# Kernel optimization log

Hardware: AMD Instinct MI355X
Metric: run time of the kernel (lower is better)

The kernel has to match this reference:

```python
import jax, jax.numpy as jnp
import numpy as np

K = 16  # kNN neighbors (KnnEncoder default)


def _bn(h, g, s):
    # eval-mode BatchNorm with running mean 0 / var 1 folded into affine
    return h * g + s


def setup_inputs() -> dict:
    key = jax.random.key(0)
    cnt = [0]
    def nk():
        cnt[0] += 1
        return jax.random.fold_in(key, cnt[0])
    B, N = 4, 4096
    def W(i, o):
        return jax.random.normal(nk(), (i, o), jnp.float32) / np.float32(i) ** 0.5
    def bias(d):
        return jnp.zeros((d,), jnp.float32)
    def gamma(d):
        return jnp.ones((d,), jnp.float32) + 0.1 * jax.random.normal(nk(), (d,), jnp.float32)
    def beta(d):
        return 0.1 * jax.random.normal(nk(), (d,), jnp.float32)
    inp = dict(
        pos=jax.random.normal(nk(), (B, N, 3), jnp.float32),
        query_point_idx=jax.random.randint(nk(), (B,), 0, N),
        # PointNetConv local MLP: 6 -> 64 -> 128 -> 256 (plain last)
        cw1=W(6, 64), cb1=bias(64), cg1=gamma(64), cs1=beta(64),
        cw2=W(64, 128), cb2=bias(128), cg2=gamma(128), cs2=beta(128),
        cw3=W(128, 256), cb3=bias(256),
        # GlobalSAModule MLP: 259 -> 256 -> 512 -> 1024 (plain last)
        sw1=W(259, 256), sb1=bias(256), sg1=gamma(256), ss1=beta(256),
        sw2=W(256, 512), sb2=bias(512), sg2=gamma(512), ss2=beta(512),
        sw3=W(512, 1024), sb3=bias(1024),
        # EdgeGraspPredictor: 1280 -> 512 -> 256 -> 16
        pw1=W(1280, 512), pb1=bias(512),
        pw2=W(512, 256), pb2=bias(256),
        pw3=W(256, 16), pb3=bias(16),
    )
    return inp


def reference(pos, query_point_idx, cw1, cb1, cg1, cs1, cw2, cb2, cg2, cs2, cw3, cb3,
              sw1, sb1, sg1, ss1, sw2, sb2, sg2, ss2, sw3, sb3,
              pw1, pb1, pw2, pb2, pw3, pb3):
    B, N, _ = pos.shape
    # kNN within each cloud (self included, as torch_geometric knn with x==y)
    d2 = jnp.sum((pos[:, :, None, :] - pos[:, None, :, :]) ** 2, axis=-1)  # [B,N,N]
    _, idx = jax.lax.top_k(-d2, K)  # [B,N,K] targets for each source point n
    nbr = jax.vmap(lambda p, i: p[i])(pos, idx)  # [B,N,K,3] target positions
    # PointNetConv message: cat([x_j = pos_src, pos_src - pos_tgt])
    src = jnp.broadcast_to(pos[:, :, None, :], (B, N, K, 3))
    h = jnp.concatenate([src, src - nbr], axis=-1)  # [B,N,K,6]
    h = jnp.maximum(_bn(h @ cw1 + cb1, cg1, cs1), 0.0)
    h = jnp.maximum(_bn(h @ cw2 + cb2, cg2, cs2), 0.0)
    m = h @ cw3 + cb3  # [B,N,K,256] per-edge messages
    # scatter-max aggregation at target nodes (every node has its self edge)
    tgt = (idx + (jnp.arange(B) * N)[:, None, None]).reshape(-1)
    x = jax.ops.segment_max(m.reshape(-1, m.shape[-1]), tgt, num_segments=B * N)
    x = x.reshape(B, N, -1)  # [B,N,256] per-point features
    # GlobalSAModule: pointwise MLP then global max pool per cloud
    g = jnp.concatenate([x, pos], axis=-1)  # [B,N,259]
    g = jnp.maximum(_bn(g @ sw1 + sb1, sg1, ss1), 0.0)
    g = jnp.maximum(_bn(g @ sw2 + sb2, sg2, ss2), 0.0)
    g = g @ sw3 + sb3  # [B,N,1024]
    scene = jnp.max(g, axis=1)  # [B,1024]
    # gather query point feature, concat with scene feature, predictor MLP
    q = query_point_idx + jnp.arange(B) * N
    point_feat = x.reshape(B * N, -1)[q]  # [B,256]
    ef = jnp.concatenate([point_feat, scene], axis=-1)  # [B,1280]
    h = jnp.maximum(ef @ pw1 + pb1, 0.0)
    h = jnp.maximum(h @ pw2 + pb2, 0.0)
    return h @ pw3 + pb3  # [B,16]
```

## Files before the change

kernel.cpp:

```cpp
#include <hip/hip_runtime.h>

#define BB 4
#define NN 4096
#define KK 16

typedef unsigned short u16;
typedef unsigned int   u32;
typedef unsigned long long u64;

typedef __attribute__((ext_vector_type(8))) short bf16x8;
typedef __attribute__((ext_vector_type(4))) float f32x4;

__device__ __forceinline__ float b2f(u16 x){ return __uint_as_float(((u32)x) << 16); }
__device__ __forceinline__ u16 f2b(float f){
    u32 u = __float_as_uint(f);
    u32 r = (u + 0x7FFFu + ((u >> 16) & 1u)) >> 16;
    return (u16)r;
}
__device__ __forceinline__ u32 fmap(float f){
    u32 u = __float_as_uint(f);
    return (u & 0x80000000u) ? ~u : (u | 0x80000000u);
}
__device__ __forceinline__ float funmap(u32 u){
    u32 v = (u & 0x80000000u) ? (u ^ 0x80000000u) : ~u;
    return __uint_as_float(v);
}

#define N_ARR 27
__device__ const int ASZ[N_ARR] = {
    49152, 384, 64, 64, 64, 8192, 128, 128, 128, 32768, 256,
    66304, 256, 256, 256, 131072, 512, 512, 512, 524288, 1024,
    655360, 512, 131072, 256, 4096, 16 };
__device__ const int AOFF[N_ARR] = {
    0, 49152, 49536, 49600, 49664, 49728, 57920, 58048, 58176, 58304, 91072,
    91328, 157632, 157888, 158144, 158400, 289472, 289984, 290496, 291008, 815296,
    816320, 1471680, 1472192, 1603264, 1603520, 1607616 };

struct Ptrs { const void* p[N_ARR]; };

#define O_POS 0
#define O_CW1 49152
#define O_CB1 49536
#define O_CG1 49600
#define O_CS1 49664
#define O_CW2 49728
#define O_CB2 57920
#define O_CG2 58048
#define O_CS2 58176
#define O_CW3 58304
#define O_CB3 91072
#define O_SW1 91328
#define O_SB1 157632
#define O_SG1 157888
#define O_SS1 158144
#define O_SW2 158400
#define O_SB2 289472
#define O_SG2 289984
#define O_SS2 290496
#define O_SW3 291008
#define O_SB3 815296
#define O_PW1 816320
#define O_PB1 1471680
#define O_PW2 1472192
#define O_PB2 1603264
#define O_PW3 1603520
#define O_PB3 1607616

__global__ void detect_kernel(const u16* __restrict__ pos_u16, u32* __restrict__ flag){
    __shared__ int cnt;
    if (threadIdx.x == 0) cnt = 0;
    __syncthreads();
    int c = 0;
    #pragma unroll
    for (int s = 0; s < 4; ++s){
        u16 u = pos_u16[2*(threadIdx.x*4 + s)];
        int e = (u >> 7) & 0xFF;
        c += (e >= 0x68 && e <= 0x82) ? 1 : 0;
    }
    atomicAdd(&cnt, c);
    __syncthreads();
    if (threadIdx.x == 0) *flag = (cnt >= 512) ? 1u : 0u;
}

__device__ __forceinline__ void pack_one_src(const void* __restrict__ src, bool isbf,
                                             u16* __restrict__ dst, int tot, int log2n,
                                             int g, int T){
    const int nmask = (1 << log2n) - 1;
    for (int id = g; id < tot; id += T){
        int i = id & 7, lg = (id >> 3) & 3;
        int rest = id >> 5;
        int n = rest & nmask;
        int ks = rest >> log2n;
        int si = (ks*32 + lg*8 + i) << log2n | n;
        dst[id] = isbf ? ((const u16*)src)[si] : f2b(((const float*)src)[si]);
    }
}

__global__ __launch_bounds__(256) void prep_kernel(Ptrs pt, const u32* __restrict__ flagp,
        float* __restrict__ dst,
        u16* __restrict__ wp2, u16* __restrict__ wp3,
        u16* __restrict__ swp1, u16* __restrict__ swp2, u16* __restrict__ swp3){
    const bool isbf = (*flagp != 0);
    const int T = gridDim.x * 256;
    const int g = blockIdx.x * 256 + threadIdx.x;
    #pragma unroll
    for (int a = 0; a < N_ARR; ++a){
        const int sz = ASZ[a], off = AOFF[a];
        if (isbf){
            const u16* s = (const u16*)pt.p[a];
            for (int i = g; i < sz; i += T) dst[off + i] = b2f(s[i]);
        } else {
            const float* s = (const float*)pt.p[a];
            for (int i = g; i < sz; i += T) dst[off + i] = s[i];
        }
    }
    pack_one_src(pt.p[5],  isbf, wp2,    8192,  7, g, T);
    pack_one_src(pt.p[9],  isbf, wp3,   32768,  8, g, T);
    pack_one_src(pt.p[11], isbf, swp1,  65536,  8, g, T);
    pack_one_src(pt.p[15], isbf, swp2, 131072,  9, g, T);
    pack_one_src(pt.p[19], isbf, swp3, 524288, 10, g, T);
}

#define QCAP 192
__device__ __forceinline__ void refine16(u64* __restrict__ buf, int& cnt, float& tau, int lane){
    u64 loc[3];
    #pragma unroll
    for (int q = 0; q < 3; ++q){
        int p = lane + (q << 6);
        loc[q] = (p < cnt) ? buf[p] : ~0ull;
    }
    u64 m = ~0ull;
    #pragma unroll
    for (int r = 0; r < KK; ++r){
        m = loc[0];
        m = loc[1] < m ? loc[1] : m;
        m = loc[2] < m ? loc[2] : m;
        #pragma unroll
        for (int off = 32; off > 0; off >>= 1){
            u64 o = __shfl_xor(m, off);
            m = o < m ? o : m;
        }
        if (lane == r) buf[r] = m;
        #pragma unroll
        for (int q = 0; q < 3; ++q) if (loc[q] == m) loc[q] = ~0ull;
    }
    cnt = KK;
    tau = __uint_as_float((u32)(m >> 32));
}

__global__ __launch_bounds__(512) void knn_kernel(const float* __restrict__ conv,
                                                  int* __restrict__ knn_out,
                                                  u32* __restrict__ deg){
    __shared__ __align__(16) u64 kbuf[16*QCAP];
    const int b  = blockIdx.x >> 8;
    const int i0 = (blockIdx.x & 255) << 4;
    const float* pb = conv + O_POS + (size_t)b*NN*3;
    const int tid = threadIdx.x;
    const int lane = tid & 63;
    const int wv = tid >> 6;
    const int iA = i0 + wv*2, iB = iA + 1;
    const float ax = pb[3*iA], ay = pb[3*iA+1], az = pb[3*iA+2];
    const float bx = pb[3*iB], by = pb[3*iB+1], bz = pb[3*iB+2];
    u64* bufA = kbuf + (wv*2)*QCAP;
    u64* bufB = bufA + QCAP;

    float tauA = 3.0e38f, tauB = 3.0e38f;
    int cntA = 0, cntB = 0;
    for (int t = 0; t < 64; t += 4){
        float cx[4], cy[4], cz[4];
        #pragma unroll
        for (int c = 0; c < 4; ++c){
            int j = lane + ((t + c) << 6);
            const float* p = pb + 3*j;
            cx[c] = p[0]; cy[c] = p[1]; cz[c] = p[2];
        }
        #pragma unroll
        for (int c = 0; c < 4; ++c){
            int j = lane + ((t + c) << 6);
            float dxA = ax - cx[c], dyA = ay - cy[c], dzA = az - cz[c];
            float d2A = __fadd_rn(__fadd_rn(__fmul_rn(dxA,dxA), __fmul_rn(dyA,dyA)), __fmul_rn(dzA,dzA));
            float dxB = bx - cx[c], dyB = by - cy[c], dzB = bz - cz[c];
            float d2B = __fadd_rn(__fadd_rn(__fmul_rn(dxB,dxB), __fmul_rn(dyB,dyB)), __fmul_rn(dzB,dzB));
            bool pA = (d2A <= tauA);
            u64 balA = __ballot(pA);
            if (balA){
                int nins = __popcll(balA);
                if (cntA + nins > QCAP) refine16(bufA, cntA, tauA, lane);
                if (pA){
                    int ofs = __popcll(balA & ((1ull << lane) - 1ull));
                    bufA[cntA + ofs] = (((u64)__float_as_uint(d2A)) << 32) | (u32)j;
                }
                cntA += nins;
            }
            bool pB = (d2B <= tauB);
            u64 balB = __ballot(pB);
            if (balB){
                int nins = __popcll(balB);
                if (cntB + nins > QCAP) refine16(bufB, cntB, tauB, lane);
                if (pB){
                    int ofs = __popcll(balB & ((1ull << lane) - 1ull));
                    bufB[cntB + ofs] = (((u64)__float_as_uint(d2B)) << 32) | (u32)j;
                }
                cntB += nins;
            }
        }
    }
    refine16(bufA, cntA, tauA, lane);
    refine16(bufB, cntB, tauB, lane);
    if (lane < KK){
        u64 kA = bufA[lane];
        int jA = (int)(u32)(kA & 0xFFFFFFFFu);
        knn_out[((size_t)(b*NN + iA))*KK + lane] = jA;
        atomicAdd(deg + (b << 12) + jA, 1u);
        u64 kB = bufB[lane];
        int jB = (int)(u32)(kB & 0xFFFFFFFFu);
        knn_out[((size_t)(b*NN + iB))*KK + lane] = jB;
        atomicAdd(deg + (b << 12) + jB, 1u);
    }
}

__global__ __launch_bounds__(1024) void scan_kernel(const u32* __restrict__ deg,
                                                    int* __restrict__ rowstart, u32* __restrict__ cursor){
    __shared__ int lsum[1024];
    const int tid = threadIdx.x;
    const int base = tid * 16;
    int loc[16]; int s = 0;
    #pragma unroll
    for (int q = 0; q < 16; ++q){ loc[q] = (int)deg[base+q]; s += loc[q]; }
    lsum[tid] = s;
    __syncthreads();
    int acc = s;
    for (int ofs = 1; ofs < 1024; ofs <<= 1){
        int t = (tid >= ofs) ? lsum[tid-ofs] : 0;
        __syncthreads();
        acc += t; lsum[tid] = acc;
        __syncthreads();
    }
    int excl = acc - s;
    #pragma unroll
    for (int q = 0; q < 16; ++q){
        rowstart[base+q] = excl; cursor[base+q] = (u32)excl; excl += loc[q];
    }
    if (tid == 1023) rowstart[16384] = excl;
}

__global__ __launch_bounds__(256) void fill_kernel(const int* __restrict__ knn,
                                                   u32* __restrict__ cursor, int* __restrict__ csr){
    int e = blockIdx.x*256 + threadIdx.x;
    int b = e >> 16;
    int t = (b << 12) + knn[e];
    u32 pos = atomicAdd(cursor + t, 1u);
    csr[pos] = e;
}

__device__ __forceinline__ bf16x8 ldfrag(const u16* h, int row, int kofs, int rowstride){
    u32 byte = (u32)((row*rowstride + kofs)*2) ^ (u32)((row & 7) << 4);
    return *(const bf16x8*)((const char*)h + byte);
}
__device__ __forceinline__ void st16(u16* h, int row, int col, int rowstride, float v){
    u32 byte = (u32)((row*rowstride + col)*2) ^ (u32)((row & 7) << 4);
    *(u16*)((char*)h + byte) = f2b(v);
}

__global__ __launch_bounds__(256, 2) void edge_kernel(
    const float* __restrict__ conv, const int* __restrict__ knn,
    const int* __restrict__ rowstart, const int* __restrict__ csr,
    const u16* __restrict__ wp2, const u16* __restrict__ wp3,
    u16* __restrict__ xh)
{
    __shared__ float in6[6][64];
    __shared__ int   lts[64];
    __shared__ int   rs_l[17];
    __shared__ float scw1[384];
    __shared__ float sc1[64], sh1[64];
    __shared__ __align__(16) u16 h1s[64*64];
    __shared__ __align__(16) u16 h2s[64*128];
    __shared__ u32 lsx[16*256];

    const float* posf = conv + O_POS;
    const float* cb1 = conv + O_CB1; const float* cg1 = conv + O_CG1; const float* cs1 = conv + O_CS1;

    const int tid = threadIdx.x;
    const int w   = tid >> 6;
    const int l   = tid & 63;
    const int t0  = blockIdx.x << 4;
    const int b   = t0 >> 12;

    if (tid < 64){ float g1 = cg1[tid]; sc1[tid]=g1; sh1[tid]=cb1[tid]*g1 + cs1[tid]; }
    if (tid < 17) rs_l[tid] = rowstart[t0 + tid];
    for (int u = tid; u < 384; u += 256) scw1[u] = conv[O_CW1 + u];
    #pragma unroll
    for (int q = 0; q < 16; ++q) lsx[q*256 + tid] = 0u;

    const int lr = l & 15, lg = l >> 4;
    const int colb2 = w << 5;
    const int colb3 = w << 6;

    float sc2v[2], sh2v[2], bs3v[4];
    #pragma unroll
    for (int nt = 0; nt < 2; ++nt){
        int c = colb2 + nt*16 + lr;
        float g2 = conv[O_CG2 + c];
        sc2v[nt] = g2; sh2v[nt] = conv[O_CB2 + c]*g2 + conv[O_CS2 + c];
    }
    #pragma unroll
    for (int nt = 0; nt < 4; ++nt) bs3v[nt] = conv[O_CB3 + colb3 + nt*16 + lr];

    __syncthreads();
    const int segstart = rs_l[0], segend = rs_l[16];
    const int nchunk = (segend - segstart + 63) >> 6;

    int curl = -1;
    float run[4];
    #pragma unroll
    for (int nt = 0; nt < 4; ++nt) run[nt] = 0.f;

    for (int ch = 0; ch < nchunk; ++ch){
        __syncthreads();
        if (tid < 64){
            int gpos = segstart + (ch << 6) + tid;
            int lt = -1;
            float ax=0,ay=0,az=0,dx=0,dy=0,dz=0;
            if (gpos < segend){
                lt = 0;
                #pragma unroll
                for (int q = 1; q < 16; ++q) lt += (gpos >= rs_l[q]) ? 1 : 0;
                int e = csr[gpos];
                int i = (e >> 4) & (NN - 1);
                int j = knn[e];
                const float* pi = posf + ((size_t)(b*NN + i))*3;
                const float* pj = posf + ((size_t)(b*NN + j))*3;
                ax = pi[0]; ay = pi[1]; az = pi[2];
                dx = ax - pj[0]; dy = ay - pj[1]; dz = az - pj[2];
            }
            lts[tid] = lt;
            in6[0][tid]=ax; in6[1][tid]=ay; in6[2][tid]=az;
            in6[3][tid]=dx; in6[4][tid]=dy; in6[5][tid]=dz;
        }
        __syncthreads();

        {
            const int e = tid & 63, c0g = (tid >> 6) << 4;
            float a0=in6[0][e], a1=in6[1][e], a2=in6[2][e],
                  a3=in6[3][e], a4=in6[4][e], a5=in6[5][e];
            u32 pk[8];
            #pragma unroll
            for (int ci = 0; ci < 16; ++ci){
                int cc = c0g + ci;
                float acc = a0*scw1[cc]     + a1*scw1[64+cc]  + a2*scw1[128+cc]
                          + a3*scw1[192+cc] + a4*scw1[256+cc] + a5*scw1[320+cc];
                float v = fmaxf(acc*sc1[cc] + sh1[cc], 0.f);
                u32 h = (u32)f2b(v);
                if (ci & 1) pk[ci >> 1] |= h << 16; else pk[ci >> 1] = h;
            }
            u32 base = (u32)(e*128 + c0g*2);
            u32 swz  = (u32)((e & 7) << 4);
            *(uint4*)((char*)h1s + (base ^ swz))        = make_uint4(pk[0],pk[1],pk[2],pk[3]);
            *(uint4*)((char*)h1s + ((base + 16) ^ swz)) = make_uint4(pk[4],pk[5],pk[6],pk[7]);
        }
        __syncthreads();

        {
            f32x4 acc2[4][2];
            #pragma unroll
            for (int mt = 0; mt < 4; ++mt)
                #pragma unroll
                for (int nt = 0; nt < 2; ++nt) acc2[mt][nt] = (f32x4){0.f,0.f,0.f,0.f};
            #pragma unroll
            for (int ks = 0; ks < 2; ++ks){
                bf16x8 bf[2];
                #pragma unroll
                for (int nt = 0; nt < 2; ++nt)
                    bf[nt] = *(const bf16x8*)(wp2 + (((ks*128 + colb2 + nt*16 + lr) << 2) + lg)*8);
                #pragma unroll
                for (int mt = 0; mt < 4; ++mt){
                    bf16x8 a = ldfrag(h1s, mt*16 + lr, ks*32 + lg*8, 64);
                    #pragma unroll
                    for (int nt = 0; nt < 2; ++nt)
                        acc2[mt][nt] = __builtin_amdgcn_mfma_f32_16x16x32_bf16(a, bf[nt], acc2[mt][nt], 0, 0, 0);
                }
            }
            #pragma unroll
            for (int mt = 0; mt < 4; ++mt)
                #pragma unroll
                for (int nt = 0; nt < 2; ++nt)
                    #pragma unroll
                    for (int r = 0; r < 4; ++r){
                        int row = mt*16 + lg*4 + r;
                        float v = fmaxf(acc2[mt][nt][r]*sc2v[nt] + sh2v[nt], 0.f);
                        st16(h2s, row, colb2 + nt*16 + lr, 128, v);
                    }
        }
        __syncthreads();

        {
            f32x4 acc3[4][4];
            #pragma unroll
            for (int mt = 0; mt < 4; ++mt)
                #pragma unroll
                for (int nt = 0; nt < 4; ++nt) acc3[mt][nt] = (f32x4){0.f,0.f,0.f,0.f};
            #pragma unroll
            for (int ks = 0; ks < 4; ++ks){
                bf16x8 bf[4];
                #pragma unroll
                for (int nt = 0; nt < 4; ++nt)
                    bf[nt] = *(const bf16x8*)(wp3 + (((ks*256 + colb3 + nt*16 + lr) << 2) + lg)*8);
                #pragma unroll
                for (int mt = 0; mt < 4; ++mt){
                    bf16x8 a = ldfrag(h2s, mt*16 + lr, ks*32 + lg*8, 128);
                    #pragma unroll
                    for (int nt = 0; nt < 4; ++nt)
                        acc3[mt][nt] = __builtin_amdgcn_mfma_f32_16x16x32_bf16(a, bf[nt], acc3[mt][nt], 0, 0, 0);
                }
            }
            #pragma unroll
            for (int mt = 0; mt < 4; ++mt)
                #pragma unroll
                for (int r = 0; r < 4; ++r){
                    int row = mt*16 + lg*4 + r;
                    int lt = lts[row];
                    if (lt != curl){
                        if (curl >= 0){
                            #pragma unroll
                            for (int nt = 0; nt < 4; ++nt)
                                atomicMax(&lsx[curl*256 + colb3 + nt*16 + lr], fmap(run[nt]));
                        }
                        curl = lt;
                        #pragma unroll
                        for (int nt = 0; nt < 4; ++nt) run[nt] = acc3[mt][nt][r] + bs3v[nt];
                    } else {
                        #pragma unroll
                        for (int nt = 0; nt < 4; ++nt) run[nt] = fmaxf(run[nt], acc3[mt][nt][r] + bs3v[nt]);
                    }
                }
        }
    }
    if (curl >= 0){
        #pragma unroll
        for (int nt = 0; nt < 4; ++nt)
            atomicMax(&lsx[curl*256 + colb3 + nt*16 + lr], fmap(run[nt]));
    }
    __syncthreads();
    #pragma unroll
    for (int q = 0; q < 16; ++q)
        xh[((size_t)(t0+q))*256 + tid] = f2b(funmap(lsx[q*256 + tid]));
}

__global__ __launch_bounds__(256, 2) void sa_kernel(
    const float* __restrict__ conv, const u16* __restrict__ xh,
    const u16* __restrict__ swp1, const u16* __restrict__ swp2, const u16* __restrict__ swp3,
    u32* __restrict__ scene_map)
{
    __shared__ __align__(16) u16 a0s[32*256];
    __shared__ __align__(16) u16 h1s[32*256];
    __shared__ __align__(16) u16 h2s[32*512];
    __shared__ float spw[3][256];
    __shared__ float spx[32], spy[32], spz[32];

    const int tid = threadIdx.x;
    const int w   = tid >> 6;
    const int l   = tid & 63;
    const int lr  = l & 15, lg = l >> 4;
    const int b   = blockIdx.x >> 7;
    const int n0  = (blockIdx.x & 127) << 5;

    #pragma unroll
    for (int it = 0; it < 4; ++it){
        int slot = it*256 + tid;
        int row = slot >> 5, ch0 = (slot & 31) << 3;
        uint4 v = *(const uint4*)(xh + ((size_t)(b*NN + n0 + row))*256 + ch0);
        *(uint4*)((char*)a0s + ((u32)(row*512 + ch0*2) ^ (u32)((row & 7) << 4))) = v;
    }
    if (tid < 96){
        int p = tid & 31, d = tid >> 5;
        float v = conv[O_POS + ((size_t)(b*NN + n0 + p))*3 + d];
        if (d == 0) spx[p] = v; else if (d == 1) spy[p] = v; else spz[p] = v;
    }
    for (int u = tid; u < 768; u += 256)
        spw[u >> 8][u & 255] = conv[O_SW1 + (256 + (u >> 8))*256 + (u & 255)];
    __syncthreads();

    {
        const int c0 = w << 6;
        float sc1v[4], sh1v[4];
        #pragma unroll
        for (int nt = 0; nt < 4; ++nt){
            int cc = c0 + nt*16 + lr;
            float g = conv[O_SG1 + cc];
            sc1v[nt] = g; sh1v[nt] = conv[O_SB1 + cc]*g + conv[O_SS1 + cc];
        }
        f32x4 acc[2][4];
        #pragma unroll
        for (int mt = 0; mt < 2; ++mt)
            #pragma unroll
            for (int nt = 0; nt < 4; ++nt)
                #pragma unroll
                for (int r = 0; r < 4; ++r){
                    int row = mt*16 + lg*4 + r;
                    int cc  = c0 + nt*16 + lr;
                    acc[mt][nt][r] = spx[row]*spw[0][cc] + spy[row]*spw[1][cc] + spz[row]*spw[2][cc];
                }
        #pragma unroll
        for (int ks = 0; ks < 8; ++ks){
            bf16x8 bf[4];
            #pragma unroll
            for (int nt = 0; nt < 4; ++nt)
                bf[nt] = *(const bf16x8*)(swp1 + (((ks*256 + c0 + nt*16 + lr) << 2) + lg)*8);
            #pragma unroll
            for (int mt = 0; mt < 2; ++mt){
                bf16x8 a = ldfrag(a0s, mt*16 + lr, ks*32 + lg*8, 256);
                #pragma unroll
                for (int nt = 0; nt < 4; ++nt)
                    acc[mt][nt] = __builtin_amdgcn_mfma_f32_16x16x32_bf16(a, bf[nt], acc[mt][nt], 0, 0, 0);
            }
        }
        #pragma unroll
        for (int mt = 0; mt < 2; ++mt)
            #pragma unroll
            for (int nt = 0; nt < 4; ++nt)
                #pragma unroll
                for (int r = 0; r < 4; ++r){
                    int row = mt*16 + lg*4 + r;
                    float v = fmaxf(acc[mt][nt][r]*sc1v[nt] + sh1v[nt], 0.f);
                    st16(h1s, row, c0 + nt*16 + lr, 256, v);
                }
    }
    __syncthreads();

    {
        const int c0 = w << 7;
        float sc2v[8], sh2v[8];
        #pragma unroll
        for (int nt = 0; nt < 8; ++nt){
            int cc = c0 + nt*16 + lr;
            float g = conv[O_SG2 + cc];
            sc2v[nt] = g; sh2v[nt] = conv[O_SB2 + cc]*g + conv[O_SS2 + cc];
        }
        f32x4 acc[2][8];
        #pragma unroll
        for (int mt = 0; mt < 2; ++mt)
            #pragma unroll
            for (int nt = 0; nt < 8; ++nt) acc[mt][nt] = (f32x4){0.f,0.f,0.f,0.f};
        #pragma unroll
        for (int ks = 0; ks < 8; ++ks){
            bf16x8 bf[8];
            #pragma unroll
            for (int nt = 0; nt < 8; ++nt)
                bf[nt] = *(const bf16x8*)(swp2 + (((ks*512 + c0 + nt*16 + lr) << 2) + lg)*8);
            #pragma unroll
            for (int mt = 0; mt < 2; ++mt){
                bf16x8 a = ldfrag(h1s, mt*16 + lr, ks*32 + lg*8, 256);
                #pragma unroll
                for (int nt = 0; nt < 8; ++nt)
                    acc[mt][nt] = __builtin_amdgcn_mfma_f32_16x16x32_bf16(a, bf[nt], acc[mt][nt], 0, 0, 0);
            }
        }
        #pragma unroll
        for (int mt = 0; mt < 2; ++mt)
            #pragma unroll
            for (int nt = 0; nt < 8; ++nt)
                #pragma unroll
                for (int r = 0; r < 4; ++r){
                    int row = mt*16 + lg*4 + r;
                    float v = fmaxf(acc[mt][nt][r]*sc2v[nt] + sh2v[nt], 0.f);
                    st16(h2s, row, c0 + nt*16 + lr, 512, v);
                }
    }
    __syncthreads();

    #pragma unroll
    for (int half = 0; half < 2; ++half){
        const int c0 = (half << 9) + (w << 7);
        f32x4 acc[2][8];
        #pragma unroll
        for (int mt = 0; mt < 2; ++mt)
            #pragma unroll
            for (int nt = 0; nt < 8; ++nt) acc[mt][nt] = (f32x4){0.f,0.f,0.f,0.f};
        #pragma unroll
        for (int ks = 0; ks < 16; ++ks){
            bf16x8 bf[8];
            #pragma unroll
            for (int nt = 0; nt < 8; ++nt)
                bf[nt] = *(const bf16x8*)(swp3 + (((ks*1024 + c0 + nt*16 + lr) << 2) + lg)*8);
            #pragma unroll
            for (int mt = 0; mt < 2; ++mt){
                bf16x8 a = ldfrag(h2s, mt*16 + lr, ks*32 + lg*8, 512);
                #pragma unroll
                for (int nt = 0; nt < 8; ++nt)
                    acc[mt][nt] = __builtin_amdgcn_mfma_f32_16x16x32_bf16(a, bf[nt], acc[mt][nt], 0, 0, 0);
            }
        }
        #pragma unroll
        for (int nt = 0; nt < 8; ++nt){
            float v = acc[0][nt][0];
            #pragma unroll
            for (int mt = 0; mt < 2; ++mt)
                #pragma unroll
                for (int r = 0; r < 4; ++r) v = fmaxf(v, acc[mt][nt][r]);
            v = fmaxf(v, __shfl_xor(v, 16));
            v = fmaxf(v, __shfl_xor(v, 32));
            if (lg == 0){
                int cc = c0 + nt*16 + lr;
                atomicMax(scene_map + (b << 10) + cc, fmap(v + conv[O_SB3 + cc]));
            }
        }
    }
}

__global__ __launch_bounds__(128) void head1_kernel(
    const float* __restrict__ conv,
    const u16* __restrict__ xh, const u32* __restrict__ scene_map, const int* __restrict__ qidx,
    float* __restrict__ h1out)
{
    __shared__ float ef[1280];
    const float* pw1 = conv + O_PW1; const float* pb1 = conv + O_PB1;
    const int b  = blockIdx.x >> 2;
    const int c0 = (blockIdx.x & 3) << 7;
    const int tid = threadIdx.x;
    const int q = qidx[b];
    for (int u = tid; u < 1280; u += 128){
        float v;
        if (u < 256) v = b2f(xh[(((size_t)(b*NN + q)) << 8) + u]);
        else         v = funmap(scene_map[(b << 10) + (u - 256)]);
        ef[u] = v;
    }
    __syncthreads();
    const int c = c0 + tid;
    float acc = pb1[c];
    for (int r = 0; r < 1280; ++r) acc += ef[r] * pw1[r*512 + c];
    h1out[(b << 9) + c] = fmaxf(acc, 0.f);
}

__global__ __launch_bounds__(256) void head2_kernel(
    const float* __restrict__ conv, const float* __restrict__ h1in,
    const u32* __restrict__ flagp, void* __restrict__ outv)
{
    __shared__ float h1[4][512];
    __shared__ float h2[4][256];
    const float* pw2 = conv + O_PW2; const float* pb2 = conv + O_PB2;
    const float* pw3 = conv + O_PW3; const float* pb3 = conv + O_PB3;
    const int tid = threadIdx.x;
    for (int u = tid; u < 2048; u += 256) h1[u >> 9][u & 511] = h1in[u];
    __syncthreads();
    for (int o = tid; o < 1024; o += 256){
        int b = o >> 8, c = o & 255;
        float acc = pb2[c];
        for (int r = 0; r < 512; ++r) acc += h1[b][r] * pw2[r*256 + c];
        h2[b][c] = fmaxf(acc, 0.f);
    }
    __syncthreads();
    if (tid < 64){
        int b = tid >> 4, c = tid & 15;
        float acc = pb3[c];
        for (int r = 0; r < 256; ++r) acc += h2[b][r] * pw3[r*16 + c];
        if (*flagp) ((u16*)outv)[tid] = f2b(acc);
        else        ((float*)outv)[tid] = acc;
    }
}

extern "C" void kernel_launch(void* const* d_in, const int* in_sizes, int n_in,
                              void* d_out, int out_size, void* d_ws, size_t ws_size,
                              hipStream_t stream){
    (void)in_sizes; (void)n_in; (void)out_size; (void)ws_size;
    const int* qidx = (const int*)d_in[1];

    char* ws = (char*)d_ws;
    u32*  flag      = (u32*)ws;
    float* conv     = (float*)(ws + 1024);
    u16*  wp2       = (u16*)(ws + 6432768);
    u16*  wp3       = (u16*)(ws + 6449152);
    u16*  swp1      = (u16*)(ws + 6514688);
    u16*  swp2      = (u16*)(ws + 6645760);
    u16*  swp3      = (u16*)(ws + 6907904);
    int*  knn       = (int*)(ws + 7956480);
    u32*  deg       = (u32*)(ws + 9005056);
    u32*  scene_map = (u32*)(ws + 9070592);
    int*  rowstart  = (int*)(ws + 9086976);
    u32*  cursor    = (u32*)(ws + 9152576);
    int*  csr       = (int*)(ws + 9218112);
    u16*  xh        = (u16*)(ws + 10266688);
    float* h1ws     = (float*)(ws + 18655296);

    Ptrs pt;
    pt.p[0] = d_in[0];
    for (int k = 1; k < N_ARR; ++k) pt.p[k] = d_in[k + 1];

    hipMemsetAsync(ws + 9005056, 0, 81920, stream);

    detect_kernel <<<1, 256, 0, stream>>>((const u16*)d_in[0], flag);
    prep_kernel   <<<512, 256, 0, stream>>>(pt, flag, conv, wp2, wp3, swp1, swp2, swp3);
    knn_kernel <<<1024, 512, 0, stream>>>(conv, knn, deg);
    scan_kernel<<<1, 1024, 0, stream>>>(deg, rowstart, cursor);
    fill_kernel<<<1024, 256, 0, stream>>>(knn, cursor, csr);
    edge_kernel<<<1024, 256, 0, stream>>>(conv, knn, rowstart, csr, wp2, wp3, xh);
    sa_kernel  <<<512, 256, 0, stream>>>(conv, xh, swp1, swp2, swp3, scene_map);
    head1_kernel<<<16, 128, 0, stream>>>(conv, xh, scene_map, qidx, h1ws);
    head2_kernel<<<1, 256, 0, stream>>>(conv, h1ws, flag, (void*)d_out);
}
```

Baseline: 381.3 us.

## Use SoA positions for kNN, trim prep copies, split head1 rows, tweak sa occupancy

Prep now writes positions into a structure-of-arrays buffer so the kNN kernel can do coalesced per-coordinate loads, and the kNN candidate loop is unrolled to 8 loads per step. Prep also stops copying weight arrays that only exist in packed bf16 form. In sa_kernel the shared-memory staging of the xh input tile is removed in favour of direct global fragment loads, and launch bounds are raised to 3 blocks per CU. head1 splits its reduction over rows across 4 thread groups and launches 64 blocks instead of 16 to get more parallelism. The direct global loads in sa_kernel lose the swizzled LDS reuse and may be less efficient per access.

```diff
diff --git a/kernel.cpp b/kernel.cpp
--- a/kernel.cpp
+++ b/kernel.cpp
@@ -43,21 +43,17 @@
 #define O_CB1 49536
 #define O_CG1 49600
 #define O_CS1 49664
-#define O_CW2 49728
 #define O_CB2 57920
 #define O_CG2 58048
 #define O_CS2 58176
-#define O_CW3 58304
 #define O_CB3 91072
 #define O_SW1 91328
 #define O_SB1 157632
 #define O_SG1 157888
 #define O_SS1 158144
-#define O_SW2 158400
 #define O_SB2 289472
 #define O_SG2 289984
 #define O_SS2 290496
-#define O_SW3 291008
 #define O_SB3 815296
 #define O_PW1 816320
 #define O_PB1 1471680
@@ -97,7 +93,7 @@
 }
 
 __global__ __launch_bounds__(256) void prep_kernel(Ptrs pt, const u32* __restrict__ flagp,
-        float* __restrict__ dst,
+        float* __restrict__ dst, float* __restrict__ psoa,
         u16* __restrict__ wp2, u16* __restrict__ wp3,
         u16* __restrict__ swp1, u16* __restrict__ swp2, u16* __restrict__ swp3){
     const bool isbf = (*flagp != 0);
@@ -105,6 +101,7 @@
     const int g = blockIdx.x * 256 + threadIdx.x;
     #pragma unroll
     for (int a = 0; a < N_ARR; ++a){
+        if (a == 5 || a == 9 || a == 15 || a == 19) continue;
         const int sz = ASZ[a], off = AOFF[a];
         if (isbf){
             const u16* s = (const u16*)pt.p[a];
@@ -114,6 +111,17 @@
             for (int i = g; i < sz; i += T) dst[off + i] = s[i];
         }
     }
+    for (int i = g; i < BB*NN; i += T){
+        float x, y, z;
+        if (isbf){
+            const u16* s = (const u16*)pt.p[0];
+            x = b2f(s[3*i]); y = b2f(s[3*i+1]); z = b2f(s[3*i+2]);
+        } else {
+            const float* s = (const float*)pt.p[0];
+            x = s[3*i]; y = s[3*i+1]; z = s[3*i+2];
+        }
+        psoa[i] = x; psoa[BB*NN + i] = y; psoa[2*BB*NN + i] = z;
+    }
     pack_one_src(pt.p[5],  isbf, wp2,    8192,  7, g, T);
     pack_one_src(pt.p[9],  isbf, wp3,   32768,  8, g, T);
     pack_one_src(pt.p[11], isbf, swp1,  65536,  8, g, T);
@@ -148,34 +156,35 @@
     tau = __uint_as_float((u32)(m >> 32));
 }
 
-__global__ __launch_bounds__(512) void knn_kernel(const float* __restrict__ conv,
+__global__ __launch_bounds__(512) void knn_kernel(const float* __restrict__ psoa,
                                                   int* __restrict__ knn_out,
                                                   u32* __restrict__ deg){
     __shared__ __align__(16) u64 kbuf[16*QCAP];
     const int b  = blockIdx.x >> 8;
     const int i0 = (blockIdx.x & 255) << 4;
-    const float* pb = conv + O_POS + (size_t)b*NN*3;
+    const float* px = psoa + b*NN;
+    const float* py = psoa + BB*NN + b*NN;
+    const float* pz = psoa + 2*BB*NN + b*NN;
     const int tid = threadIdx.x;
     const int lane = tid & 63;
     const int wv = tid >> 6;
     const int iA = i0 + wv*2, iB = iA + 1;
-    const float ax = pb[3*iA], ay = pb[3*iA+1], az = pb[3*iA+2];
-    const float bx = pb[3*iB], by = pb[3*iB+1], bz = pb[3*iB+2];
+    const float ax = px[iA], ay = py[iA], az = pz[iA];
+    const float bx = px[iB], by = py[iB], bz = pz[iB];
     u64* bufA = kbuf + (wv*2)*QCAP;
     u64* bufB = bufA + QCAP;
 
     float tauA = 3.0e38f, tauB = 3.0e38f;
     int cntA = 0, cntB = 0;
-    for (int t = 0; t < 64; t += 4){
-        float cx[4], cy[4], cz[4];
-        #pragma unroll
-        for (int c = 0; c < 4; ++c){
+    for (int t = 0; t < 64; t += 8){
+        float cx[8], cy[8], cz[8];
+        #pragma unroll
+        for (int c = 0; c < 8; ++c){
             int j = lane + ((t + c) << 6);
-            const float* p = pb + 3*j;
-            cx[c] = p[0]; cy[c] = p[1]; cz[c] = p[2];
-        }
-        #pragma unroll
-        for (int c = 0; c < 4; ++c){
+            cx[c] = px[j]; cy[c] = py[j]; cz[c] = pz[j];
+        }
+        #pragma unroll
+        for (int c = 0; c < 8; ++c){
             int j = lane + ((t + c) << 6);
             float dxA = ax - cx[c], dyA = ay - cy[c], dzA = az - cz[c];
             float d2A = __fadd_rn(__fadd_rn(__fmul_rn(dxA,dxA), __fmul_rn(dyA,dyA)), __fmul_rn(dzA,dzA));
@@ -446,12 +455,11 @@
         xh[((size_t)(t0+q))*256 + tid] = f2b(funmap(lsx[q*256 + tid]));
 }
 
-__global__ __launch_bounds__(256, 2) void sa_kernel(
+__global__ __launch_bounds__(256, 3) void sa_kernel(
     const float* __restrict__ conv, const u16* __restrict__ xh,
     const u16* __restrict__ swp1, const u16* __restrict__ swp2, const u16* __restrict__ swp3,
     u32* __restrict__ scene_map)
 {
-    __shared__ __align__(16) u16 a0s[32*256];
     __shared__ __align__(16) u16 h1s[32*256];
     __shared__ __align__(16) u16 h2s[32*512];
     __shared__ float spw[3][256];
@@ -463,14 +471,8 @@
     const int lr  = l & 15, lg = l >> 4;
     const int b   = blockIdx.x >> 7;
     const int n0  = (blockIdx.x & 127) << 5;
-
-    #pragma unroll
-    for (int it = 0; it < 4; ++it){
-        int slot = it*256 + tid;
-        int row = slot >> 5, ch0 = (slot & 31) << 3;
-        uint4 v = *(const uint4*)(xh + ((size_t)(b*NN + n0 + row))*256 + ch0);
-        *(uint4*)((char*)a0s + ((u32)(row*512 + ch0*2) ^ (u32)((row & 7) << 4))) = v;
-    }
+    const u16* xrow = xh + ((size_t)(b*NN + n0))*256;
+
     if (tid < 96){
         int p = tid & 31, d = tid >> 5;
         float v = conv[O_POS + ((size_t)(b*NN + n0 + p))*3 + d];
@@ -508,7 +510,7 @@
                 bf[nt] = *(const bf16x8*)(swp1 + (((ks*256 + c0 + nt*16 + lr) << 2) + lg)*8);
             #pragma unroll
             for (int mt = 0; mt < 2; ++mt){
-                bf16x8 a = ldfrag(a0s, mt*16 + lr, ks*32 + lg*8, 256);
+                bf16x8 a = *(const bf16x8*)(xrow + (mt*16 + lr)*256 + ks*32 + lg*8);
                 #pragma unroll
                 for (int nt = 0; nt < 4; ++nt)
                     acc[mt][nt] = __builtin_amdgcn_mfma_f32_16x16x32_bf16(a, bf[nt], acc[mt][nt], 0, 0, 0);
@@ -613,9 +615,10 @@
     float* __restrict__ h1out)
 {
     __shared__ float ef[1280];
+    __shared__ float psum[4][32];
     const float* pw1 = conv + O_PW1; const float* pb1 = conv + O_PB1;
-    const int b  = blockIdx.x >> 2;
-    const int c0 = (blockIdx.x & 3) << 7;
+    const int b  = blockIdx.x >> 4;
+    const int c0 = (blockIdx.x & 15) << 5;
     const int tid = threadIdx.x;
     const int q = qidx[b];
     for (int u = tid; u < 1280; u += 128){
@@ -625,10 +628,16 @@
         ef[u] = v;
     }
     __syncthreads();
-    const int c = c0 + tid;
-    float acc = pb1[c];
-    for (int r = 0; r < 1280; ++r) acc += ef[r] * pw1[r*512 + c];
-    h1out[(b << 9) + c] = fmaxf(acc, 0.f);
+    const int c = c0 + (tid & 31);
+    const int rc = tid >> 5;
+    float acc = 0.f;
+    for (int r = rc*320; r < rc*320 + 320; ++r) acc += ef[r] * pw1[r*512 + c];
+    psum[rc][tid & 31] = acc;
+    __syncthreads();
+    if (tid < 32){
+        float a = psum[0][tid] + psum[1][tid] + psum[2][tid] + psum[3][tid] + pb1[c0 + tid];
+        h1out[(b << 9) + c0 + tid] = fmaxf(a, 0.f);
+    }
 }
 
 __global__ __launch_bounds__(256) void head2_kernel(
@@ -680,6 +689,7 @@
     int*  csr       = (int*)(ws + 9218112);
     u16*  xh        = (u16*)(ws + 10266688);
     float* h1ws     = (float*)(ws + 18655296);
+    float* psoa     = (float*)(ws + 18663488);
 
     Ptrs pt;
     pt.p[0] = d_in[0];
@@ -688,12 +698,12 @@
     hipMemsetAsync(ws + 9005056, 0, 81920, stream);
 
     detect_kernel <<<1, 256, 0, stream>>>((const u16*)d_in[0], flag);
-    prep_kernel   <<<512, 256, 0, stream>>>(pt, flag, conv, wp2, wp3, swp1, swp2, swp3);
-    knn_kernel <<<1024, 512, 0, stream>>>(conv, knn, deg);
+    prep_kernel   <<<512, 256, 0, stream>>>(pt, flag, conv, psoa, wp2, wp3, swp1, swp2, swp3);
+    knn_kernel <<<1024, 512, 0, stream>>>(psoa, knn, deg);
     scan_kernel<<<1, 1024, 0, stream>>>(deg, rowstart, cursor);
     fill_kernel<<<1024, 256, 0, stream>>>(knn, cursor, csr);
     edge_kernel<<<1024, 256, 0, stream>>>(conv, knn, rowstart, csr, wp2, wp3, xh);
     sa_kernel  <<<512, 256, 0, stream>>>(conv, xh, swp1, swp2, swp3, scene_map);
-    head1_kernel<<<16, 128, 0, stream>>>(conv, xh, scene_map, qidx, h1ws);
+    head1_kernel<<<64, 128, 0, stream>>>(conv, xh, scene_map, qidx, h1ws);
     head2_kernel<<<1, 256, 0, stream>>>(conv, h1ws, flag, (void*)d_out);
 }
```

Result: faster. 371.0 us (-2.7%).
